# Optimization experiments

Hardware: AMD Instinct MI355X
Metric: run time of the kernel (lower is better)

The kernel has to match this reference:

```python
import jax, jax.numpy as jnp
import numpy as np

B, TQ, TM, D, ATTN, H = 8, 1024, 1024, 512, 512, 8
HEAD_DIM = ATTN // H
TEMPERATURE = 1.0
CAUSALITY = True
NEG_INF = -2.0 ** 32 + 1


def setup_inputs() -> dict:
    key = jax.random.key(0)
    ks = jax.random.split(key, 7)
    scale = 1.0 / np.sqrt(D)
    return {
        "inputs": jax.random.normal(ks[0], (B, TQ, D), dtype=jnp.float32),
        "memory": jax.random.normal(ks[1], (B, TM, D), dtype=jnp.float32),
        "Wq": jax.random.normal(ks[2], (D, ATTN), dtype=jnp.float32) * scale,
        "Wk": jax.random.normal(ks[3], (D, ATTN), dtype=jnp.float32) * scale,
        "Wv": jax.random.normal(ks[4], (D, ATTN), dtype=jnp.float32) * scale,
        "memory_lengths": jax.random.randint(ks[5], (B,), TM // 2, TM + 1, dtype=jnp.int32),
        "query_lengths": jax.random.randint(ks[6], (B,), TQ // 2, TQ + 1, dtype=jnp.int32),
    }


def _split_head(x):
    # [B, T, ATTN] -> [B, H, T, HEAD_DIM]
    b, t, _ = x.shape
    return x.reshape(b, t, H, HEAD_DIM).transpose(0, 2, 1, 3)


def reference(inputs, memory, Wq, Wk, Wv, memory_lengths, query_lengths):
    q = _split_head(inputs @ Wq)   # [B,H,Tq,hd]
    k = _split_head(memory @ Wk)   # [B,H,Tm,hd]
    v = _split_head(memory @ Wv)   # [B,H,Tm,hd]

    logits = jnp.einsum("bhqd,bhmd->bhqm", q, k)
    logits = logits / jnp.sqrt(jnp.float32(HEAD_DIM)) / TEMPERATURE

    mem_mask = jnp.arange(TM)[None, :] < memory_lengths[:, None]   # [B,Tm]
    qry_mask = jnp.arange(TQ)[None, :] < query_lengths[:, None]    # [B,Tq]
    length_mask = qry_mask[:, :, None] & mem_mask[:, None, :]      # [B,Tq,Tm]
    mask = length_mask[:, None, :, :]                              # [B,1,Tq,Tm]
    if CAUSALITY:
        causal = jnp.tril(jnp.ones((TQ, TM), dtype=bool))
        mask = mask & causal[None, None, :, :]

    logits = jnp.where(mask, logits, jnp.float32(NEG_INF))
    alignments = jax.nn.softmax(logits, axis=3)                    # [B,H,Tq,Tm]
    contexts = jnp.einsum("bhqm,bhmd->bhqd", alignments, v)
    contexts = contexts.transpose(0, 2, 1, 3).reshape(inputs.shape[0], TQ, ATTN)
    return contexts, alignments
```

## Files before the change

### kernel.cpp

```cpp
#include <hip/hip_runtime.h>

#define NB 8
#define NTQ 1024
#define NTM 1024
#define ND 512
#define NATTN 512
#define NH 8
#define NDH 64

typedef _Float16 half8 __attribute__((ext_vector_type(8)));
typedef float f32x4 __attribute__((ext_vector_type(4)));

__global__ __launch_bounds__(256) void wprep_kernel(
    const float* __restrict__ Wq, const float* __restrict__ Wk,
    const float* __restrict__ Wv, _Float16* __restrict__ Wt) {
  const int z = blockIdx.z;
  const float* __restrict__ W = (z == 0) ? Wq : ((z == 1) ? Wk : Wv);
  _Float16* __restrict__ out = Wt + (size_t)z * NATTN * ND;
  const int k0 = blockIdx.x * 64;
  const int n0 = blockIdx.y * 64;
  __shared__ __align__(16) _Float16 Ls[64][72];
  const int t = threadIdx.x;
  const int sr = t >> 2, sc = (t & 3) * 16;
  const float4* src = (const float4*)(W + (size_t)(k0 + sr) * NATTN + n0 + sc);
  float4 f0 = src[0], f1 = src[1], f2 = src[2], f3 = src[3];
  float gv[16];
  *(float4*)&gv[0] = f0; *(float4*)&gv[4] = f1;
  *(float4*)&gv[8] = f2; *(float4*)&gv[12] = f3;
#pragma unroll
  for (int j = 0; j < 16; j++) Ls[sc + j][sr] = (_Float16)gv[j];
  __syncthreads();
  _Float16* dst = out + (size_t)(n0 + sr) * ND + k0 + sc;
  *(half8*)dst = *(const half8*)&Ls[sr][sc];
  *(half8*)(dst + 8) = *(const half8*)&Ls[sr][sc + 8];
}

__global__ __launch_bounds__(256) void proj_kernel(
    const float* __restrict__ inputs, const float* __restrict__ memory,
    const _Float16* __restrict__ Wt, _Float16* __restrict__ Qh,
    _Float16* __restrict__ Kh, _Float16* __restrict__ Vth) {
  const int id = blockIdx.x;
  const int xcd = id & 7;
  const int g = id >> 3;
  const int z = g >> 6;
  const int gg = g & 63;
  const int row0 = (xcd * 16 + (gg >> 2)) * 64;
  const int col0 = (gg & 3) * 128;

  const float* __restrict__ A = (z == 0) ? inputs : memory;
  const _Float16* __restrict__ Wz = Wt + (size_t)z * NATTN * ND;

  __shared__ __align__(16) _Float16 pool[64 * 72 + 128 * 72];
  _Float16* Asb = pool;
  _Float16* Wsb = pool + 64 * 72;

  const int t = threadIdx.x;
  const int w = t >> 6, L = t & 63;
  const int lrow = L & 15, quad = L >> 4;
  const int sr = t >> 2, sc = (t & 3) * 16;
  const int sr2 = t >> 1, sc2 = (t & 1) * 32;

  const f32x4 zf = {0.f, 0.f, 0.f, 0.f};
  f32x4 acc[8];
#pragma unroll
  for (int i = 0; i < 8; i++) acc[i] = zf;

  for (int k0 = 0; k0 < ND; k0 += 64) {
    {
      const float4* src = (const float4*)(A + (size_t)(row0 + sr) * ND + k0 + sc);
      float4 f0 = src[0], f1 = src[1], f2 = src[2], f3 = src[3];
      half8 h0, h1;
      h0[0] = (_Float16)f0.x; h0[1] = (_Float16)f0.y; h0[2] = (_Float16)f0.z; h0[3] = (_Float16)f0.w;
      h0[4] = (_Float16)f1.x; h0[5] = (_Float16)f1.y; h0[6] = (_Float16)f1.z; h0[7] = (_Float16)f1.w;
      h1[0] = (_Float16)f2.x; h1[1] = (_Float16)f2.y; h1[2] = (_Float16)f2.z; h1[3] = (_Float16)f2.w;
      h1[4] = (_Float16)f3.x; h1[5] = (_Float16)f3.y; h1[6] = (_Float16)f3.z; h1[7] = (_Float16)f3.w;
      *(half8*)&Asb[sr * 72 + sc] = h0;
      *(half8*)&Asb[sr * 72 + sc + 8] = h1;
    }
    {
      const half8* wsrc = (const half8*)(Wz + (size_t)(col0 + sr2) * ND + k0 + sc2);
#pragma unroll
      for (int j = 0; j < 4; j++) *(half8*)&Wsb[sr2 * 72 + sc2 + 8 * j] = wsrc[j];
    }
    __syncthreads();
#pragma unroll
    for (int ks = 0; ks < 2; ks++) {
      half8 a = *(const half8*)&Asb[(w * 16 + lrow) * 72 + ks * 32 + quad * 8];
#pragma unroll
      for (int nt = 0; nt < 8; nt++) {
        half8 b = *(const half8*)&Wsb[(nt * 16 + lrow) * 72 + ks * 32 + quad * 8];
        acc[nt] = __builtin_amdgcn_mfma_f32_16x16x32_f16(a, b, acc[nt], 0, 0, 0);
      }
    }
    __syncthreads();
  }

  const int bb = row0 >> 10;
  const int tr0 = row0 & 1023;
  const int hh0 = col0 >> 6;

  if (z <= 1) {
#pragma unroll
    for (int nt = 0; nt < 8; nt++)
#pragma unroll
      for (int r = 0; r < 4; r++)
        pool[(w * 16 + quad * 4 + r) * 136 + nt * 16 + lrow] = (_Float16)acc[nt][r];
    __syncthreads();
    const int sce = (t & 3) * 32;
    _Float16* base = (z == 0) ? Qh : Kh;
    _Float16* dst = base + (size_t)(bb * NH + hh0 + (sce >> 6)) * NTQ * NDH +
                    (size_t)(tr0 + sr) * NDH + (sce & 63);
#pragma unroll
    for (int j = 0; j < 4; j++)
      *(half8*)(dst + 8 * j) = *(const half8*)&pool[sr * 136 + sce + 8 * j];
  } else {
#pragma unroll
    for (int nt = 0; nt < 8; nt++)
#pragma unroll
      for (int r = 0; r < 4; r++)
        Wsb[(nt * 16 + lrow) * 72 + w * 16 + quad * 4 + r] = (_Float16)acc[nt][r];
    __syncthreads();
    _Float16* dst = Vth +
        ((size_t)(bb * NH + hh0 + (sr2 >> 6)) * NDH + (sr2 & 63)) * NTM + tr0 + sc2;
#pragma unroll
    for (int j = 0; j < 4; j++)
      *(half8*)(dst + 8 * j) = *(const half8*)&Wsb[sr2 * 72 + sc2 + 8 * j];
  }
}

__global__ __launch_bounds__(256) void attn_kernel(
    const _Float16* __restrict__ Qh, const _Float16* __restrict__ Kh,
    const _Float16* __restrict__ Vth, const int* __restrict__ mem_len,
    const int* __restrict__ qry_len, float* __restrict__ ctx_out,
    float* __restrict__ align_out) {
  const int bh = blockIdx.x;
  const int qt = blockIdx.y;
  const int bb = bh >> 3;
  const int hh = bh & 7;
  const int q0 = qt * 64;

  __shared__ __align__(16) _Float16 Qs[64][72];
  __shared__ __align__(16) _Float16 Ks[64][72];
  __shared__ __align__(16) _Float16 Vts[64][72];
  __shared__ __align__(16) _Float16 Ps[4][16][72];
  __shared__ float vsum_lds[64];

  const int t = threadIdx.x, w = t >> 6, L = t & 63;
  const int lrow = L & 15, quad = L >> 4;
  const int qlen = qry_len[bb], mlen = mem_len[bb];
  const int mtop = (mlen + 63) >> 6;
  const bool has_causal = q0 < qlen;
  const bool has_uniform = (q0 + 64) > qlen;
  const int n_comp = has_causal ? min(qt + 1, mtop) : 0;
  const _Float16* Qbase = Qh + (size_t)bh * NTQ * NDH;
  const _Float16* Kbase = Kh + (size_t)bh * NTM * NDH;
  const _Float16* Vbase = Vth + (size_t)bh * NDH * NTM;
  const int sr = t >> 2, sc = (t & 3) * 16;
  const f32x4 zf = {0.f, 0.f, 0.f, 0.f};
  float* abase = align_out + (size_t)bh * NTQ * NTM;
  float* cbase = ctx_out + (size_t)bb * NTQ * NATTN + (size_t)hh * NDH;

  if (has_causal) {
    if (n_comp < 16) {
      const int c0 = n_comp * 64;
      const int row = q0 + sr;
      if (row < qlen) {
        float* rp = abase + (size_t)row * NTM;
        const float4 z4 = {0.f, 0.f, 0.f, 0.f};
        for (int c = c0 + (t & 3) * 4; c < NTM; c += 16) *(float4*)(rp + c) = z4;
      }
    }
    {
      const half8* src = (const half8*)(Qbase + (size_t)(q0 + sr) * NDH + sc);
      *(half8*)&Qs[sr][sc] = src[0];
      *(half8*)&Qs[sr][sc + 8] = src[1];
    }
    const int qg = q0 + w * 16 + quad * 4;
    float rowsum[4] = {0.f, 0.f, 0.f, 0.f};
    __syncthreads();

    for (int mt = 0; mt < n_comp; mt++) {
      {
        const half8* src = (const half8*)(Kbase + (size_t)(mt * 64 + sr) * NDH + sc);
        *(half8*)&Ks[sr][sc] = src[0];
        *(half8*)&Ks[sr][sc + 8] = src[1];
      }
      __syncthreads();
      f32x4 sacc[4];
#pragma unroll
      for (int i = 0; i < 4; i++) sacc[i] = zf;
#pragma unroll
      for (int ks = 0; ks < 2; ks++) {
        half8 a = *(const half8*)&Qs[w * 16 + lrow][ks * 32 + quad * 8];
#pragma unroll
        for (int nt = 0; nt < 4; nt++) {
          half8 b = *(const half8*)&Ks[nt * 16 + lrow][ks * 32 + quad * 8];
          sacc[nt] = __builtin_amdgcn_mfma_f32_16x16x32_f16(a, b, sacc[nt], 0, 0, 0);
        }
      }
#pragma unroll
      for (int nt = 0; nt < 4; nt++) {
        int m = mt * 64 + nt * 16 + lrow;
#pragma unroll
        for (int r = 0; r < 4; r++) {
          int q = qg + r;
          float p;
          if (q >= qlen) p = 0.0f;
          else if (m > q || m >= mlen) p = 0.0f;
          else p = __expf(sacc[nt][r] * 0.125f);
          rowsum[r] += p;
        }
      }
      __syncthreads();
    }
    float inv[4];
#pragma unroll
    for (int r = 0; r < 4; r++) {
      float s = rowsum[r];
      s += __shfl_xor(s, 1, 16);
      s += __shfl_xor(s, 2, 16);
      s += __shfl_xor(s, 4, 16);
      s += __shfl_xor(s, 8, 16);
      inv[r] = 1.0f / s;
    }

    f32x4 cacc[4];
#pragma unroll
    for (int i = 0; i < 4; i++) cacc[i] = zf;

    for (int mt = 0; mt < n_comp; mt++) {
      {
        const half8* src = (const half8*)(Kbase + (size_t)(mt * 64 + sr) * NDH + sc);
        *(half8*)&Ks[sr][sc] = src[0];
        *(half8*)&Ks[sr][sc + 8] = src[1];
        const half8* vsrc = (const half8*)(Vbase + (size_t)sr * NTM + mt * 64 + sc);
        *(half8*)&Vts[sr][sc] = vsrc[0];
        *(half8*)&Vts[sr][sc + 8] = vsrc[1];
      }
      __syncthreads();
      f32x4 sacc[4];
#pragma unroll
      for (int i = 0; i < 4; i++) sacc[i] = zf;
#pragma unroll
      for (int ks = 0; ks < 2; ks++) {
        half8 a = *(const half8*)&Qs[w * 16 + lrow][ks * 32 + quad * 8];
#pragma unroll
        for (int nt = 0; nt < 4; nt++) {
          half8 b = *(const half8*)&Ks[nt * 16 + lrow][ks * 32 + quad * 8];
          sacc[nt] = __builtin_amdgcn_mfma_f32_16x16x32_f16(a, b, sacc[nt], 0, 0, 0);
        }
      }
#pragma unroll
      for (int nt = 0; nt < 4; nt++) {
        int m = mt * 64 + nt * 16 + lrow;
#pragma unroll
        for (int r = 0; r < 4; r++) {
          int q = qg + r;
          float p;
          if (q >= qlen) p = 0.0f;
          else if (m > q || m >= mlen) p = 0.0f;
          else p = __expf(sacc[nt][r] * 0.125f) * inv[r];
          if (q < qlen) abase[(size_t)q * NTM + m] = p;
          Ps[w][quad * 4 + r][nt * 16 + lrow] = (_Float16)p;
        }
      }
#pragma unroll
      for (int ks = 0; ks < 2; ks++) {
        half8 a = *(const half8*)&Ps[w][lrow][ks * 32 + quad * 8];
#pragma unroll
        for (int dt = 0; dt < 4; dt++) {
          half8 b = *(const half8*)&Vts[dt * 16 + lrow][ks * 32 + quad * 8];
          cacc[dt] = __builtin_amdgcn_mfma_f32_16x16x32_f16(a, b, cacc[dt], 0, 0, 0);
        }
      }
      __syncthreads();
    }

#pragma unroll
    for (int dt = 0; dt < 4; dt++) {
#pragma unroll
      for (int r = 0; r < 4; r++) {
        int q = qg + r;
        if (q < qlen) cbase[(size_t)q * NATTN + dt * 16 + lrow] = cacc[dt][r];
      }
    }
  }

  if (has_uniform) {
    const int d = t >> 2;
    const int seg = t & 3;
    const _Float16* vp = Vbase + (size_t)d * NTM + seg * 256;
    float s = 0.f;
#pragma unroll
    for (int j = 0; j < 32; j++) {
      half8 v = *(const half8*)(vp + 8 * j);
#pragma unroll
      for (int e = 0; e < 8; e++) s += (float)v[e];
    }
    s += __shfl_xor(s, 1, 4);
    s += __shfl_xor(s, 2, 4);
    if (seg == 0) vsum_lds[d] = s * (1.0f / 1024.0f);
    __syncthreads();
    const int qu0 = (q0 > qlen) ? q0 : qlen;
    for (int q = qu0 + w; q < q0 + 64; q += 4)
      cbase[(size_t)q * NATTN + L] = vsum_lds[L];
    const float cval = 1.0f / 1024.0f;
    const f32x4 c4 = {cval, cval, cval, cval};
    for (int q = qu0 + w; q < q0 + 64; q += 4) {
      float* rp = abase + (size_t)q * NTM + L * 4;
#pragma unroll
      for (int j = 0; j < 4; j++) *(f32x4*)(rp + j * 256) = c4;
    }
  }
}

extern "C" void kernel_launch(void* const* d_in, const int* in_sizes, int n_in,
                              void* d_out, int out_size, void* d_ws,
                              size_t ws_size, hipStream_t stream) {
  const float* inputs = (const float*)d_in[0];
  const float* memory = (const float*)d_in[1];
  const float* Wq = (const float*)d_in[2];
  const float* Wk = (const float*)d_in[3];
  const float* Wv = (const float*)d_in[4];
  const int* mlen = (const int*)d_in[5];
  const int* qlen = (const int*)d_in[6];

  float* ctx = (float*)d_out;
  float* align = ctx + (size_t)NB * NTQ * NATTN;

  _Float16* Qh = (_Float16*)d_ws;
  _Float16* Kh = Qh + (size_t)NB * NH * NTQ * NDH;
  _Float16* Vth = Kh + (size_t)NB * NH * NTM * NDH;
  _Float16* Wt = (_Float16*)align;

  wprep_kernel<<<dim3(8, 8, 3), 256, 0, stream>>>(Wq, Wk, Wv, Wt);
  proj_kernel<<<dim3(1536), 256, 0, stream>>>(inputs, memory, Wt, Qh, Kh, Vth);
  attn_kernel<<<dim3(64, 16), 256, 0, stream>>>(Qh, Kh, Vth, mlen, qlen, ctx,
                                                align);
}
```

Before: 384.2 us.

## Keep Q fragments in registers and register-prefetch next K/V tiles

Removes the Q shared-memory tile and has each lane load its Q MFMA fragments straight from global memory into registers once. In both the rowsum pass and the output pass, the next K (and V) tile is loaded into registers right after the barrier, so the global load overlaps the current tile's MFMA and softmax work. This cuts LDS traffic and one barrier, and hides global latency, at the cost of extra registers that may lower occupancy. The kernel is likely dominated by the large fp32 alignment writes, so the benefit may be limited.

```diff
diff --git a/kernel.cpp b/kernel.cpp
--- a/kernel.cpp
+++ b/kernel.cpp
@@ -139,7 +139,6 @@
   const int hh = bh & 7;
   const int q0 = qt * 64;
 
-  __shared__ __align__(16) _Float16 Qs[64][72];
   __shared__ __align__(16) _Float16 Ks[64][72];
   __shared__ __align__(16) _Float16 Vts[64][72];
   __shared__ __align__(16) _Float16 Ps[4][16][72];
@@ -170,33 +169,35 @@
         for (int c = c0 + (t & 3) * 4; c < NTM; c += 16) *(float4*)(rp + c) = z4;
       }
     }
-    {
-      const half8* src = (const half8*)(Qbase + (size_t)(q0 + sr) * NDH + sc);
-      *(half8*)&Qs[sr][sc] = src[0];
-      *(half8*)&Qs[sr][sc + 8] = src[1];
-    }
+    const int qrow = q0 + w * 16 + lrow;
+    const half8 qa0 = *(const half8*)(Qbase + (size_t)qrow * NDH + quad * 8);
+    const half8 qa1 = *(const half8*)(Qbase + (size_t)qrow * NDH + 32 + quad * 8);
     const int qg = q0 + w * 16 + quad * 4;
     float rowsum[4] = {0.f, 0.f, 0.f, 0.f};
-    __syncthreads();
-
+
+    half8 kr0, kr1;
+    {
+      const half8* src = (const half8*)(Kbase + (size_t)sr * NDH + sc);
+      kr0 = src[0]; kr1 = src[1];
+    }
     for (int mt = 0; mt < n_comp; mt++) {
-      {
-        const half8* src = (const half8*)(Kbase + (size_t)(mt * 64 + sr) * NDH + sc);
-        *(half8*)&Ks[sr][sc] = src[0];
-        *(half8*)&Ks[sr][sc + 8] = src[1];
-      }
+      *(half8*)&Ks[sr][sc] = kr0;
+      *(half8*)&Ks[sr][sc + 8] = kr1;
       __syncthreads();
+      if (mt + 1 < n_comp) {
+        const half8* src =
+            (const half8*)(Kbase + (size_t)((mt + 1) * 64 + sr) * NDH + sc);
+        kr0 = src[0]; kr1 = src[1];
+      }
       f32x4 sacc[4];
 #pragma unroll
       for (int i = 0; i < 4; i++) sacc[i] = zf;
 #pragma unroll
-      for (int ks = 0; ks < 2; ks++) {
-        half8 a = *(const half8*)&Qs[w * 16 + lrow][ks * 32 + quad * 8];
-#pragma unroll
-        for (int nt = 0; nt < 4; nt++) {
-          half8 b = *(const half8*)&Ks[nt * 16 + lrow][ks * 32 + quad * 8];
-          sacc[nt] = __builtin_amdgcn_mfma_f32_16x16x32_f16(a, b, sacc[nt], 0, 0, 0);
-        }
+      for (int nt = 0; nt < 4; nt++) {
+        half8 b0 = *(const half8*)&Ks[nt * 16 + lrow][quad * 8];
+        half8 b1 = *(const half8*)&Ks[nt * 16 + lrow][32 + quad * 8];
+        sacc[nt] = __builtin_amdgcn_mfma_f32_16x16x32_f16(qa0, b0, sacc[nt], 0, 0, 0);
+        sacc[nt] = __builtin_amdgcn_mfma_f32_16x16x32_f16(qa1, b1, sacc[nt], 0, 0, 0);
       }
 #pragma unroll
       for (int nt = 0; nt < 4; nt++) {
@@ -228,27 +229,36 @@
 #pragma unroll
     for (int i = 0; i < 4; i++) cacc[i] = zf;
 
+    half8 vr0, vr1;
+    {
+      const half8* ksrc = (const half8*)(Kbase + (size_t)sr * NDH + sc);
+      kr0 = ksrc[0]; kr1 = ksrc[1];
+      const half8* vsrc = (const half8*)(Vbase + (size_t)sr * NTM + sc);
+      vr0 = vsrc[0]; vr1 = vsrc[1];
+    }
     for (int mt = 0; mt < n_comp; mt++) {
-      {
-        const half8* src = (const half8*)(Kbase + (size_t)(mt * 64 + sr) * NDH + sc);
-        *(half8*)&Ks[sr][sc] = src[0];
-        *(half8*)&Ks[sr][sc + 8] = src[1];
-        const half8* vsrc = (const half8*)(Vbase + (size_t)sr * NTM + mt * 64 + sc);
-        *(half8*)&Vts[sr][sc] = vsrc[0];
-        *(half8*)&Vts[sr][sc + 8] = vsrc[1];
-      }
+      *(half8*)&Ks[sr][sc] = kr0;
+      *(half8*)&Ks[sr][sc + 8] = kr1;
+      *(half8*)&Vts[sr][sc] = vr0;
+      *(half8*)&Vts[sr][sc + 8] = vr1;
       __syncthreads();
+      if (mt + 1 < n_comp) {
+        const half8* ksrc =
+            (const half8*)(Kbase + (size_t)((mt + 1) * 64 + sr) * NDH + sc);
+        kr0 = ksrc[0]; kr1 = ksrc[1];
+        const half8* vsrc =
+            (const half8*)(Vbase + (size_t)sr * NTM + (mt + 1) * 64 + sc);
+        vr0 = vsrc[0]; vr1 = vsrc[1];
+      }
       f32x4 sacc[4];
 #pragma unroll
       for (int i = 0; i < 4; i++) sacc[i] = zf;
 #pragma unroll
-      for (int ks = 0; ks < 2; ks++) {
-        half8 a = *(const half8*)&Qs[w * 16 + lrow][ks * 32 + quad * 8];
-#pragma unroll
-        for (int nt = 0; nt < 4; nt++) {
-          half8 b = *(const half8*)&Ks[nt * 16 + lrow][ks * 32 + quad * 8];
-          sacc[nt] = __builtin_amdgcn_mfma_f32_16x16x32_f16(a, b, sacc[nt], 0, 0, 0);
-        }
+      for (int nt = 0; nt < 4; nt++) {
+        half8 b0 = *(const half8*)&Ks[nt * 16 + lrow][quad * 8];
+        half8 b1 = *(const half8*)&Ks[nt * 16 + lrow][32 + quad * 8];
+        sacc[nt] = __builtin_amdgcn_mfma_f32_16x16x32_f16(qa0, b0, sacc[nt], 0, 0, 0);
+        sacc[nt] = __builtin_amdgcn_mfma_f32_16x16x32_f16(qa1, b1, sacc[nt], 0, 0, 0);
       }
 #pragma unroll
       for (int nt = 0; nt < 4; nt++) {
```

After: 382.0 us. No clear change (-0.6%).
